# Kernel optimization log

Hardware: AMD Instinct MI355X
Metric: run time of the kernel (lower is better)

## Reference

```python
import jax, jax.numpy as jnp
import numpy as np

TOP_K = 2

def setup_inputs() -> dict:
    key = jax.random.key(0)
    ks = jax.random.split(key, 8)
    B, S, D, E = 2, 2048, 1024, 8
    F = 4 * D
    x = jax.random.normal(ks[0], (B, S, D), dtype=jnp.float32)
    Wg = jax.random.normal(ks[1], (D, E), dtype=jnp.float32) / np.sqrt(D)
    bg = jnp.zeros((E,), dtype=jnp.float32)
    W1 = jax.random.normal(ks[2], (E, D, F), dtype=jnp.float32) / np.sqrt(D)
    b1 = jnp.zeros((E, F), dtype=jnp.float32)
    W2 = jax.random.normal(ks[3], (E, F, D), dtype=jnp.float32) / np.sqrt(F)
    b2 = jnp.zeros((E, D), dtype=jnp.float32)
    return {"x": x, "Wg": Wg, "bg": bg, "W1": W1, "b1": b1, "W2": W2, "b2": b2}

def reference(x, Wg, bg, W1, b1, W2, b2):
    B, S, D = x.shape
    T = B * S
    xf = x.reshape(T, D)
    # Router: softmax gates, top-k, scatter into sparse dispatch mask [T, E]
    gates = jax.nn.softmax(xf @ Wg + bg, axis=-1)
    topk_vals, topk_idx = jax.lax.top_k(gates, TOP_K)
    rows = jnp.arange(T)[:, None]
    mask = jnp.zeros_like(gates).at[rows, topk_idx].set(topk_vals)
    # Per-expert dense FFN over all tokens (world_size=1 bucket), masked combine
    h = jax.nn.relu(jnp.einsum('td,edf->etf', xf, W1) + b1[:, None, :])  # [E,T,4D]
    y = jnp.einsum('etf,efd->etd', h, W2) + b2[:, None, :]               # [E,T,D]
    out = jnp.einsum('te,etd->td', mask, y)                              # combine
    return out.reshape(B, S, D)
```

## Files before the change

kernel.cpp:

```cpp
#include <hip/hip_runtime.h>
#include <hip/hip_bf16.h>
#include <math.h>

typedef short short8 __attribute__((ext_vector_type(8)));
typedef short s4v __attribute__((ext_vector_type(4)));
typedef float f32x4 __attribute__((ext_vector_type(4)));
typedef unsigned short ushort4v __attribute__((ext_vector_type(4)));

#define T_TOK 4096
#define D_DIM 1024
#define E_NUM 8
#define F_DIM 4096
#define NSLOT (2 * T_TOK)

#define BM 128
#define BN 128
#define BK 32
#define GROWS 10
#define KSPL 3

#define NCONV 8192
#define NROUTB (T_TOK / 4)
#define G1BLK (8 * 32 * GROWS)
#define NGRP 64

__device__ __forceinline__ short f2bf(float f) {
  unsigned u = __builtin_bit_cast(unsigned, f);
  u = (u + 0x7FFFu + ((u >> 16) & 1u)) >> 16;
  return (short)u;
}
__device__ __forceinline__ float bf2f(unsigned short s) {
  unsigned u = ((unsigned)s) << 16;
  return __builtin_bit_cast(float, u);
}

__device__ __forceinline__ void gload_lds16(unsigned short* lds, const unsigned short* g) {
  __builtin_amdgcn_global_load_lds(
      (const __attribute__((address_space(1))) unsigned int*)g,
      (__attribute__((address_space(3))) unsigned int*)lds, 16, 0, 0);
}

#define MFMA_BF16 __builtin_amdgcn_mfma_f32_16x16x32_bf16
#define FSWZ(r) (((r) >> 1) & 3)

__device__ __forceinline__ void tconv_body(
    const float* __restrict__ ine, unsigned short* __restrict__ oute,
    int R, int C, int c0, int r0, float (*tile)[65]) {
  int tid = threadIdx.x;
  int lr = tid >> 4;
  int lc = (tid & 15) * 4;
#pragma unroll
  for (int p = 0; p < 4; ++p) {
    int row = p * 16 + lr;
    float4 v = *(const float4*)&ine[(size_t)(r0 + row) * C + c0 + lc];
    tile[row][lc] = v.x; tile[row][lc + 1] = v.y;
    tile[row][lc + 2] = v.z; tile[row][lc + 3] = v.w;
  }
  __syncthreads();
#pragma unroll
  for (int p = 0; p < 4; ++p) {
    int crow = p * 16 + lr;
    s4v o;
#pragma unroll
    for (int j = 0; j < 4; ++j) o[j] = f2bf(tile[lc + j][crow]);
    *(s4v*)&oute[(size_t)(c0 + crow) * R + r0 + lc] = o;
  }
}

__global__ __launch_bounds__(256) void pre_kernel(
    const float* __restrict__ x, const float* __restrict__ Wg,
    const float* __restrict__ bg, const float* __restrict__ W1,
    unsigned short* __restrict__ w1t,
    int* __restrict__ texp, float* __restrict__ tgate,
    unsigned short* __restrict__ xb) {
  __shared__ float tile[64][65];
  int bid = blockIdx.x;
  if (bid < NCONV) {
    int e = bid & 7;
    int q = bid >> 3;
    int c0 = (q & 63) * 64;
    int r0 = (q >> 6) * 64;
    tconv_body(W1 + (size_t)e * D_DIM * F_DIM, w1t + (size_t)e * D_DIM * F_DIM,
               D_DIM, F_DIM, c0, r0, tile);
    return;
  }
  int rb = bid - NCONV;
  int wid = threadIdx.x >> 6;
  int lane = threadIdx.x & 63;
  int t = rb * 4 + wid;

  double acc[E_NUM];
#pragma unroll
  for (int e = 0; e < E_NUM; ++e) acc[e] = 0.0;
  const float* xr = x + (size_t)t * D_DIM;
  unsigned short* xbr = xb + (size_t)t * D_DIM;
  for (int d = lane; d < D_DIM; d += 64) {
    float xf = xr[d];
    xbr[d] = (unsigned short)f2bf(xf);
    double xv = (double)xf;
#pragma unroll
    for (int e = 0; e < E_NUM; ++e) acc[e] += xv * (double)Wg[d * E_NUM + e];
  }
#pragma unroll
  for (int off = 32; off > 0; off >>= 1) {
#pragma unroll
    for (int e = 0; e < E_NUM; ++e) acc[e] += __shfl_down(acc[e], off);
  }
  if (lane == 0) {
    double lg[E_NUM];
    double m = -1e300;
#pragma unroll
    for (int e = 0; e < E_NUM; ++e) {
      lg[e] = acc[e] + (double)bg[e];
      m = fmax(m, lg[e]);
    }
    double s = 0.0;
#pragma unroll
    for (int e = 0; e < E_NUM; ++e) { lg[e] = exp(lg[e] - m); s += lg[e]; }
    int e0 = 0; double g0 = lg[0];
#pragma unroll
    for (int e = 1; e < E_NUM; ++e) if (lg[e] > g0) { g0 = lg[e]; e0 = e; }
    int e1 = -1; double g1 = -1.0;
#pragma unroll
    for (int e = 0; e < E_NUM; ++e)
      if (e != e0 && lg[e] > g1) { g1 = lg[e]; e1 = e; }
    texp[2 * t]     = e0;
    texp[2 * t + 1] = e1;
    tgate[2 * t]     = (float)(g0 / s);
    tgate[2 * t + 1] = (float)(g1 / s);
  }
}

__global__ __launch_bounds__(64) void count_kernel(
    const int* __restrict__ texp, int* __restrict__ grp_cnt, int* __restrict__ rank_of) {
  __shared__ int lcnt[E_NUM];
  int g = blockIdx.x;
  int lane = threadIdx.x;
  int t = g * 64 + lane;
  int e0 = texp[2 * t], e1 = texp[2 * t + 1];
  unsigned long long below = (1ULL << lane) - 1ULL;
  int r0 = 0, r1 = 0;
#pragma unroll
  for (int e = 0; e < E_NUM; ++e) {
    unsigned long long m0 = __ballot(e0 == e);
    unsigned long long m1 = __ballot(e1 == e);
    int c0 = __popcll(m0);
    if (e0 == e) r0 = __popcll(m0 & below);
    if (e1 == e) r1 = c0 + __popcll(m1 & below);
    if (lane == 0) lcnt[e] = c0 + __popcll(m1);
  }
  rank_of[2 * t]     = r0;
  rank_of[2 * t + 1] = r1;
  __syncthreads();
  if (lane < E_NUM) grp_cnt[g * E_NUM + lane] = lcnt[lane];
}

__global__ __launch_bounds__(64) void offsets_kernel(
    const int* __restrict__ grp_cnt, int* __restrict__ off,
    int* __restrict__ cnt, int* __restrict__ base) {
  __shared__ int tot[E_NUM], offs[E_NUM + 1];
  int lane = threadIdx.x;
  if (lane < E_NUM) {
    int s = 0;
    for (int g = 0; g < NGRP; ++g) s += grp_cnt[g * E_NUM + lane];
    tot[lane] = s;
  }
  __syncthreads();
  if (lane == 0) {
    int o = 0;
    for (int e = 0; e < E_NUM; ++e) { offs[e] = o; o += tot[e]; }
    offs[E_NUM] = o;
    for (int e = 0; e <= E_NUM; ++e) off[e] = offs[e];
    for (int e = 0; e < E_NUM; ++e) cnt[e] = tot[e];
  }
  __syncthreads();
  if (lane < E_NUM) {
    int run = offs[lane];
    for (int g = 0; g < NGRP; ++g) {
      base[g * E_NUM + lane] = run;
      run += grp_cnt[g * E_NUM + lane];
    }
  }
}

__global__ __launch_bounds__(256) void assign_kernel(
    const int* __restrict__ texp, const float* __restrict__ tgate,
    const int* __restrict__ base, const int* __restrict__ rank_of,
    int* __restrict__ tok_of, float* __restrict__ gate_of, int* __restrict__ slot_of) {
  int t = blockIdx.x * 256 + threadIdx.x;
  if (t >= T_TOK) return;
  int g = t >> 6;
#pragma unroll
  for (int k = 0; k < 2; ++k) {
    int e = texp[2 * t + k];
    int s = base[g * E_NUM + e] + rank_of[2 * t + k];
    tok_of[s] = t;
    gate_of[s] = tgate[2 * t + k];
    slot_of[2 * t + k] = s;
  }
}

__global__ __launch_bounds__(256) void tconv_kernel(
    const float* __restrict__ in, unsigned short* __restrict__ out, int R, int C) {
  __shared__ float tile[64][65];
  int e = blockIdx.z;
  tconv_body(in + (size_t)e * R * C, out + (size_t)e * R * C,
             R, C, blockIdx.x * 64, blockIdx.y * 64, tile);
}

__global__ __launch_bounds__(256, 4) void gemm1_kernel(
    const unsigned short* __restrict__ xb, const unsigned short* __restrict__ w1t,
    const float* __restrict__ b1,
    const int* __restrict__ off, const int* __restrict__ cnt,
    const int* __restrict__ tok_of, unsigned short* __restrict__ h,
    const float* __restrict__ W2src, unsigned short* __restrict__ w2dst,
    int gemm_blocks) {
  __shared__ __align__(16) char smem[4 * BM * BK * 2];
  int bid = blockIdx.x;
  if (bid >= gemm_blocks) {
    int tix = bid - gemm_blocks;
    int e = tix & 7;
    int q = tix >> 3;
    int c0 = (q & 15) * 64;
    int r0 = (q >> 4) * 64;
    float (*tile)[65] = reinterpret_cast<float(*)[65]>(smem);
    tconv_body(W2src + (size_t)e * F_DIM * D_DIM, w2dst + (size_t)e * F_DIM * D_DIM,
               F_DIM, D_DIM, c0, r0, tile);
    return;
  }
  unsigned short (*As)[BM * BK] = reinterpret_cast<unsigned short(*)[BM * BK]>(smem);
  unsigned short (*Bs)[BN * BK] = reinterpret_cast<unsigned short(*)[BN * BK]>(smem + 2 * BM * BK * 2);

  int e = bid & 7;
  int w = bid >> 3;
  int fx = w & 31;
  int ty = w >> 5;
  int count = cnt[e];
  if (ty * BM >= count) return;
  int f0 = fx * BN;
  int base = off[e] + ty * BM;

  int tid = threadIdx.x;
  int lane = tid & 63;
  int wid = tid >> 6;
  int wr = wid >> 1, wc = wid & 1;

  const unsigned short* aga[2];
  const unsigned short* bga[2];
  const unsigned short* w1e = w1t + (size_t)e * ((size_t)F_DIM * D_DIM);
#pragma unroll
  for (int i = 0; i < 2; ++i) {
    int pos = i * 256 + tid;
    int row = pos >> 2;
    int sl = (pos & 3) ^ FSWZ(row & 15);
    int idx = ty * BM + row;
    int tok = tok_of[(idx < count) ? (base + row) : off[e]];
    aga[i] = xb + (size_t)tok * D_DIM + sl * 8;
    bga[i] = w1e + (size_t)(f0 + row) * D_DIM + sl * 8;
  }

  f32x4 acc[4][4];
#pragma unroll
  for (int m = 0; m < 4; ++m)
#pragma unroll
    for (int n = 0; n < 4; ++n) acc[m][n] = (f32x4){0.f, 0.f, 0.f, 0.f};

#define STAGE1(buf, k0) do { \
    _Pragma("unroll") \
    for (int i = 0; i < 2; ++i) { \
      gload_lds16(&As[buf][(i * 256 + tid) * 8], aga[i] + (k0)); \
      gload_lds16(&Bs[buf][(i * 256 + tid) * 8], bga[i] + (k0)); \
    } \
  } while (0)

  STAGE1(0, 0);
  __syncthreads();

  int rr = lane & 15, hi = lane >> 4;
  int so = (hi ^ FSWZ(rr)) * 8;
  const int nt = D_DIM / BK;
  for (int t = 0; t < nt; ++t) {
    int b = t & 1;
    if (t + 1 < nt) STAGE1(b ^ 1, (t + 1) * BK);
    const unsigned short* ab = &As[b][0];
    const unsigned short* bb = &Bs[b][0];
    short8 af[4], bf[4];
#pragma unroll
    for (int m = 0; m < 4; ++m)
      af[m] = *(const short8*)(ab + (wr * 64 + m * 16 + rr) * 32 + so);
#pragma unroll
    for (int n = 0; n < 4; ++n)
      bf[n] = *(const short8*)(bb + (wc * 64 + n * 16 + rr) * 32 + so);
    __builtin_amdgcn_s_setprio(1);
#pragma unroll
    for (int m = 0; m < 4; ++m)
#pragma unroll
      for (int n = 0; n < 4; ++n)
        acc[m][n] = MFMA_BF16(af[m], bf[n], acc[m][n], 0, 0, 0);
    __builtin_amdgcn_s_setprio(0);
    __syncthreads();
  }
#undef STAGE1

  int col = lane & 15, rowq = (lane >> 4) * 4;
  float bias[4];
#pragma unroll
  for (int n = 0; n < 4; ++n) bias[n] = b1[e * F_DIM + f0 + wc * 64 + n * 16 + col];
#pragma unroll
  for (int m = 0; m < 4; ++m)
#pragma unroll
    for (int i = 0; i < 4; ++i) {
      int rl = wr * 64 + m * 16 + rowq + i;
      if (ty * BM + rl < count) {
        int slot = base + rl;
#pragma unroll
        for (int n = 0; n < 4; ++n) {
          int f = f0 + wc * 64 + n * 16 + col;
          float v = acc[m][n][i] + bias[n];
          h[(size_t)slot * F_DIM + f] = (unsigned short)f2bf(fmaxf(v, 0.f));
        }
      }
    }
}

__global__ __launch_bounds__(256, 4) void gemm2_kernel(
    const unsigned short* __restrict__ h, const unsigned short* __restrict__ w2t,
    const float* __restrict__ b2,
    const int* __restrict__ off, const int* __restrict__ cnt,
    unsigned short* __restrict__ yp) {
  int bid = blockIdx.x;
  int e = bid & 7;
  int w = bid >> 3;
  int kc = w % 3;
  int u = w / 3;
  int cx = u & 7;
  int ty = u >> 3;
  int count = cnt[e];
  if (ty * BM >= count) return;
  int d0 = cx * BN;
  int klo = kc * 43 * BK;
  const int nt = (kc < 2) ? 43 : 42;
  int base = off[e] + ty * BM;

  __shared__ __align__(16) unsigned short As[2][BM * BK];
  __shared__ __align__(16) unsigned short Bs[2][BN * BK];

  int tid = threadIdx.x;
  int lane = tid & 63;
  int wid = tid >> 6;
  int wr = wid >> 1, wc = wid & 1;

  const unsigned short* aga[2];
  const unsigned short* bga[2];
  const unsigned short* w2e = w2t + (size_t)e * ((size_t)D_DIM * F_DIM);
#pragma unroll
  for (int i = 0; i < 2; ++i) {
    int pos = i * 256 + tid;
    int row = pos >> 2;
    int sl = (pos & 3) ^ FSWZ(row & 15);
    int arow = base + row;
    if (arow > NSLOT - 1) arow = NSLOT - 1;
    aga[i] = h + (size_t)arow * F_DIM + klo + sl * 8;
    bga[i] = w2e + (size_t)(d0 + row) * F_DIM + klo + sl * 8;
  }

  f32x4 acc[4][4];
#pragma unroll
  for (int m = 0; m < 4; ++m)
#pragma unroll
    for (int n = 0; n < 4; ++n) acc[m][n] = (f32x4){0.f, 0.f, 0.f, 0.f};

#define STAGE2(buf, k0) do { \
    _Pragma("unroll") \
    for (int i = 0; i < 2; ++i) { \
      gload_lds16(&As[buf][(i * 256 + tid) * 8], aga[i] + (k0)); \
      gload_lds16(&Bs[buf][(i * 256 + tid) * 8], bga[i] + (k0)); \
    } \
  } while (0)

  STAGE2(0, 0);
  __syncthreads();

  int rr = lane & 15, hi = lane >> 4;
  int so = (hi ^ FSWZ(rr)) * 8;
  for (int t = 0; t < nt; ++t) {
    int b = t & 1;
    if (t + 1 < nt) STAGE2(b ^ 1, (t + 1) * BK);
    const unsigned short* ab = &As[b][0];
    const unsigned short* bb = &Bs[b][0];
    short8 af[4], bf[4];
#pragma unroll
    for (int m = 0; m < 4; ++m)
      af[m] = *(const short8*)(ab + (wr * 64 + m * 16 + rr) * 32 + so);
#pragma unroll
    for (int n = 0; n < 4; ++n)
      bf[n] = *(const short8*)(bb + (wc * 64 + n * 16 + rr) * 32 + so);
    __builtin_amdgcn_s_setprio(1);
#pragma unroll
    for (int m = 0; m < 4; ++m)
#pragma unroll
      for (int n = 0; n < 4; ++n)
        acc[m][n] = MFMA_BF16(af[m], bf[n], acc[m][n], 0, 0, 0);
    __builtin_amdgcn_s_setprio(0);
    __syncthreads();
  }
#undef STAGE2

  int col = lane & 15, rowq = (lane >> 4) * 4;
  float bias[4];
#pragma unroll
  for (int n = 0; n < 4; ++n)
    bias[n] = (kc == 0) ? b2[e * D_DIM + d0 + wc * 64 + n * 16 + col] : 0.f;
  unsigned short* ypk = yp + (size_t)kc * NSLOT * D_DIM;
#pragma unroll
  for (int m = 0; m < 4; ++m)
#pragma unroll
    for (int i = 0; i < 4; ++i) {
      int rl = wr * 64 + m * 16 + rowq + i;
      if (ty * BM + rl < count) {
        int slot = base + rl;
#pragma unroll
        for (int n = 0; n < 4; ++n) {
          int d = d0 + wc * 64 + n * 16 + col;
          float v = acc[m][n][i] + bias[n];
          ypk[(size_t)slot * D_DIM + d] = (unsigned short)f2bf(v);
        }
      }
    }
}

__global__ __launch_bounds__(256) void combine_kernel(
    const unsigned short* __restrict__ yp, const int* __restrict__ slot_of,
    const float* __restrict__ tgate, float* __restrict__ out) {
  int t = blockIdx.x;
  int d = threadIdx.x * 4;
  int s0 = slot_of[2 * t], s1 = slot_of[2 * t + 1];
  float g0 = tgate[2 * t], g1 = tgate[2 * t + 1];
  float4 o = {0.f, 0.f, 0.f, 0.f};
  float* op = (float*)&o;
#pragma unroll
  for (int kc = 0; kc < KSPL; ++kc) {
    const unsigned short* ypk = yp + (size_t)kc * NSLOT * D_DIM;
    ushort4v a = *(const ushort4v*)&ypk[(size_t)s0 * D_DIM + d];
    ushort4v b = *(const ushort4v*)&ypk[(size_t)s1 * D_DIM + d];
#pragma unroll
    for (int j = 0; j < 4; ++j)
      op[j] += g0 * bf2f(a[j]) + g1 * bf2f(b[j]);
  }
  *(float4*)&out[(size_t)t * D_DIM + d] = o;
}

extern "C" void kernel_launch(void* const* d_in, const int* in_sizes, int n_in,
                              void* d_out, int out_size, void* d_ws, size_t ws_size,
                              hipStream_t stream) {
  const float* x  = (const float*)d_in[0];
  const float* Wg = (const float*)d_in[1];
  const float* bg = (const float*)d_in[2];
  const float* W1 = (const float*)d_in[3];
  const float* b1 = (const float*)d_in[4];
  const float* W2 = (const float*)d_in[5];
  const float* b2 = (const float*)d_in[6];
  float* out = (float*)d_out;

  char* ws = (char*)d_ws;
  int*   off     = (int*)(ws + 0);
  int*   cnt     = (int*)(ws + 128);
  int*   grp_cnt = (int*)(ws + 1024);
  int*   base    = (int*)(ws + 4096);
  int*   texp    = (int*)(ws + 8192);
  float* tgate   = (float*)(ws + 8192 + NSLOT * 4);
  int*   rank_of = (int*)(ws + 8192 + NSLOT * 8);
  int*   tok_of  = (int*)(ws + 8192 + NSLOT * 12);
  float* gate_of = (float*)(ws + 8192 + NSLOT * 16);
  int*   slot_of = (int*)(ws + 8192 + NSLOT * 20);

  const size_t WSZ  = (size_t)E_NUM * D_DIM * F_DIM * 2;
  const size_t HSZ  = (size_t)NSLOT * F_DIM * 2;
  const size_t YPSZ = (size_t)KSPL * NSLOT * D_DIM * 2;
  size_t o_xb = 256 * 1024;
  size_t o_w1 = o_xb + (size_t)T_TOK * D_DIM * 2;
  bool overlap = ws_size >= o_w1 + 2 * WSZ + HSZ + YPSZ;
  size_t o_w2 = overlap ? (o_w1 + WSZ) : o_w1;
  size_t o_h  = o_w2 + WSZ;
  size_t o_yp = o_h + HSZ;

  unsigned short* xb  = (unsigned short*)(ws + o_xb);
  unsigned short* w1t = (unsigned short*)(ws + o_w1);
  unsigned short* w2t = (unsigned short*)(ws + o_w2);
  unsigned short* h   = (unsigned short*)(ws + o_h);
  unsigned short* yp  = (unsigned short*)(ws + o_yp);

  pre_kernel<<<NCONV + NROUTB, 256, 0, stream>>>(
      x, Wg, bg, W1, w1t, texp, tgate, xb);
  count_kernel<<<NGRP, 64, 0, stream>>>(texp, grp_cnt, rank_of);
  offsets_kernel<<<1, 64, 0, stream>>>(grp_cnt, off, cnt, base);
  assign_kernel<<<(T_TOK + 255) / 256, 256, 0, stream>>>(
      texp, tgate, base, rank_of, tok_of, gate_of, slot_of);

  if (overlap) {
    gemm1_kernel<<<G1BLK + NCONV, 256, 0, stream>>>(
        xb, w1t, b1, off, cnt, tok_of, h, W2, w2t, G1BLK);
  } else {
    gemm1_kernel<<<G1BLK, 256, 0, stream>>>(
        xb, w1t, b1, off, cnt, tok_of, h, W2, w2t, G1BLK);
    tconv_kernel<<<dim3(D_DIM / 64, F_DIM / 64, E_NUM), 256, 0, stream>>>(
        W2, w2t, F_DIM, D_DIM);
  }

  gemm2_kernel<<<8 * KSPL * 8 * GROWS, 256, 0, stream>>>(
      h, w2t, b2, off, cnt, yp);
  combine_kernel<<<T_TOK, 256, 0, stream>>>(yp, slot_of, tgate, out);
}
```

Before: 302.4 us.

## Use 4-way K split in gemm2, dispatch W2 conversion first, widen combine

Raises the gemm2 K-split from 3 to 4 so each chunk is an even 32 tiles and block index decoding uses shifts. This means more gemm2 blocks and one more partial buffer for combine to read. In the fused gemm1 launch, the W2 transpose-convert blocks now take the low block IDs, so they are scheduled before the GEMM blocks. The combine kernel now handles two tokens per block with 8 elements per thread. The extra partial-sum pass adds memory traffic in exchange for better load balance.

```diff
diff --git a/kernel.cpp b/kernel.cpp
--- a/kernel.cpp
+++ b/kernel.cpp
@@ -17,7 +17,7 @@
 #define BN 128
 #define BK 32
 #define GROWS 10
-#define KSPL 3
+#define KSPL 4
 
 #define NCONV 8192
 #define NROUTB (T_TOK / 4)
@@ -214,13 +214,12 @@
     const int* __restrict__ off, const int* __restrict__ cnt,
     const int* __restrict__ tok_of, unsigned short* __restrict__ h,
     const float* __restrict__ W2src, unsigned short* __restrict__ w2dst,
-    int gemm_blocks) {
+    int conv_blocks) {
   __shared__ __align__(16) char smem[4 * BM * BK * 2];
   int bid = blockIdx.x;
-  if (bid >= gemm_blocks) {
-    int tix = bid - gemm_blocks;
-    int e = tix & 7;
-    int q = tix >> 3;
+  if (bid < conv_blocks) {
+    int e = bid & 7;
+    int q = bid >> 3;
     int c0 = (q & 15) * 64;
     int r0 = (q >> 4) * 64;
     float (*tile)[65] = reinterpret_cast<float(*)[65]>(smem);
@@ -231,8 +230,9 @@
   unsigned short (*As)[BM * BK] = reinterpret_cast<unsigned short(*)[BM * BK]>(smem);
   unsigned short (*Bs)[BN * BK] = reinterpret_cast<unsigned short(*)[BN * BK]>(smem + 2 * BM * BK * 2);
 
-  int e = bid & 7;
-  int w = bid >> 3;
+  int gid = bid - conv_blocks;
+  int e = gid & 7;
+  int w = gid >> 3;
   int fx = w & 31;
   int ty = w >> 5;
   int count = cnt[e];
@@ -331,15 +331,15 @@
   int bid = blockIdx.x;
   int e = bid & 7;
   int w = bid >> 3;
-  int kc = w % 3;
-  int u = w / 3;
+  int kc = w & 3;
+  int u = w >> 2;
   int cx = u & 7;
   int ty = u >> 3;
   int count = cnt[e];
   if (ty * BM >= count) return;
   int d0 = cx * BN;
-  int klo = kc * 43 * BK;
-  const int nt = (kc < 2) ? 43 : 42;
+  int klo = kc * (F_DIM / KSPL);
+  const int nt = (F_DIM / KSPL) / BK;
   int base = off[e] + ty * BM;
 
   __shared__ __align__(16) unsigned short As[2][BM * BK];
@@ -432,22 +432,30 @@
 __global__ __launch_bounds__(256) void combine_kernel(
     const unsigned short* __restrict__ yp, const int* __restrict__ slot_of,
     const float* __restrict__ tgate, float* __restrict__ out) {
-  int t = blockIdx.x;
-  int d = threadIdx.x * 4;
+  int t = blockIdx.x * 2 + (threadIdx.x >> 7);
+  int d = (threadIdx.x & 127) * 8;
   int s0 = slot_of[2 * t], s1 = slot_of[2 * t + 1];
   float g0 = tgate[2 * t], g1 = tgate[2 * t + 1];
-  float4 o = {0.f, 0.f, 0.f, 0.f};
-  float* op = (float*)&o;
+  float o[8];
+#pragma unroll
+  for (int j = 0; j < 8; ++j) o[j] = 0.f;
 #pragma unroll
   for (int kc = 0; kc < KSPL; ++kc) {
     const unsigned short* ypk = yp + (size_t)kc * NSLOT * D_DIM;
-    ushort4v a = *(const ushort4v*)&ypk[(size_t)s0 * D_DIM + d];
-    ushort4v b = *(const ushort4v*)&ypk[(size_t)s1 * D_DIM + d];
-#pragma unroll
-    for (int j = 0; j < 4; ++j)
-      op[j] += g0 * bf2f(a[j]) + g1 * bf2f(b[j]);
-  }
-  *(float4*)&out[(size_t)t * D_DIM + d] = o;
+    ushort4v a0 = *(const ushort4v*)&ypk[(size_t)s0 * D_DIM + d];
+    ushort4v a1 = *(const ushort4v*)&ypk[(size_t)s0 * D_DIM + d + 4];
+    ushort4v b0 = *(const ushort4v*)&ypk[(size_t)s1 * D_DIM + d];
+    ushort4v b1 = *(const ushort4v*)&ypk[(size_t)s1 * D_DIM + d + 4];
+#pragma unroll
+    for (int j = 0; j < 4; ++j) {
+      o[j]     += g0 * bf2f(a0[j]) + g1 * bf2f(b0[j]);
+      o[j + 4] += g0 * bf2f(a1[j]) + g1 * bf2f(b1[j]);
+    }
+  }
+  float4 v0 = {o[0], o[1], o[2], o[3]};
+  float4 v1 = {o[4], o[5], o[6], o[7]};
+  *(float4*)&out[(size_t)t * D_DIM + d] = v0;
+  *(float4*)&out[(size_t)t * D_DIM + d + 4] = v1;
 }
 
 extern "C" void kernel_launch(void* const* d_in, const int* in_sizes, int n_in,
@@ -498,16 +506,16 @@
       texp, tgate, base, rank_of, tok_of, gate_of, slot_of);
 
   if (overlap) {
-    gemm1_kernel<<<G1BLK + NCONV, 256, 0, stream>>>(
-        xb, w1t, b1, off, cnt, tok_of, h, W2, w2t, G1BLK);
+    gemm1_kernel<<<NCONV + G1BLK, 256, 0, stream>>>(
+        xb, w1t, b1, off, cnt, tok_of, h, W2, w2t, NCONV);
   } else {
     gemm1_kernel<<<G1BLK, 256, 0, stream>>>(
-        xb, w1t, b1, off, cnt, tok_of, h, W2, w2t, G1BLK);
+        xb, w1t, b1, off, cnt, tok_of, h, W2, w2t, 0);
     tconv_kernel<<<dim3(D_DIM / 64, F_DIM / 64, E_NUM), 256, 0, stream>>>(
         W2, w2t, F_DIM, D_DIM);
   }
 
   gemm2_kernel<<<8 * KSPL * 8 * GROWS, 256, 0, stream>>>(
       h, w2t, b2, off, cnt, yp);
-  combine_kernel<<<T_TOK, 256, 0, stream>>>(yp, slot_of, tgate, out);
-}
+  combine_kernel<<<T_TOK / 2, 256, 0, stream>>>(yp, slot_of, tgate, out);
+}
```

New measurement: 321.7 us. 6.4% more time.
